# Performance work log

Measured on AMD Instinct MI355X. Metric: run time of the kernel, lower is better.

The kernel has to match this reference:

```python
import jax, jax.numpy as jnp
import numpy as np

B, N, T, CIN, HID, EMB, K = 32, 256, 13, 2, 64, 10, 2


def setup_inputs() -> dict:
    key = jax.random.key(0)
    ks = jax.random.split(key, 24)
    r = lambda i, shape, s=1.0: jax.random.normal(ks[i], shape, jnp.float32) * s
    return {
        "times": jnp.arange(T, dtype=jnp.float32),
        # natural cubic spline coefficients: (B, N, T-1, CIN)
        "coeff_a": r(0, (B, N, T - 1, CIN)),
        "coeff_b": r(1, (B, N, T - 1, CIN), 0.1),
        "coeff_two_c": r(2, (B, N, T - 1, CIN), 0.1),
        "coeff_three_d": r(3, (B, N, T - 1, CIN), 0.1),
        # initial_h / initial_z linear layers (input -> hidden)
        "W_h": r(4, (CIN, HID), 0.5), "b_h": r(5, (HID,), 0.1),
        "W_z": r(6, (CIN, HID), 0.5), "b_z": r(7, (HID,), 0.1),
        # func_f (FinalTanh_f): linear_in, one hidden linear, linear_out -> hidden*input
        "Wf_in": r(8, (HID, HID), 0.1), "bf_in": r(9, (HID,), 0.05),
        "Wf_hid": r(10, (HID, HID), 0.1), "bf_hid": r(11, (HID,), 0.05),
        "Wf_out": r(12, (HID, HID * CIN), 0.1), "bf_out": r(13, (HID * CIN,), 0.05),
        # func_g (VectorField_g, g_type='agc')
        "Wg_in": r(14, (HID, HID), 0.1), "bg_in": r(15, (HID,), 0.05),
        "Eg": r(16, (N, EMB)),
        "W_pool": r(17, (EMB, K, HID, HID), 0.1),
        "b_pool": r(18, (EMB, HID), 0.1),
        "Wg_out": r(19, (HID, HID * CIN), 0.1), "bg_out": r(20, (HID * CIN,), 0.05),
    }


def reference(times, coeff_a, coeff_b, coeff_two_c, coeff_three_d,
              W_h, b_h, W_z, b_z,
              Wf_in, bf_in, Wf_hid, bf_hid, Wf_out, bf_out,
              Wg_in, bg_in, Eg, W_pool, b_pool, Wg_out, bg_out):
    maxidx = coeff_b.shape[-2] - 1

    def dX_dt(t):  # NaturalCubicSpline.derivative
        idx = jnp.clip(jnp.searchsorted(times, t, side='right') - 1, 0, maxidx)
        frac = t - times[idx]
        b = coeff_b[..., idx, :]
        c = coeff_two_c[..., idx, :]
        d = coeff_three_d[..., idx, :]
        return b + (c + d * frac) * frac  # (B, N, CIN)

    # adaptive graph conv (agc) static pieces, cheb_k = 2
    A = jax.nn.softmax(jax.nn.relu(Eg @ Eg.T), axis=1)          # (N, N)
    supports = jnp.stack([jnp.eye(N, dtype=A.dtype), A])        # (K, N, N)
    Wn = jnp.einsum('nd,dkio->nkio', Eg, W_pool)                # (N, K, HID, HID)
    bn = Eg @ b_pool                                            # (N, HID)

    def func_f(h):  # FinalTanh_f: MLP -> (B, N, HID, CIN) field
        x = jax.nn.relu(h @ Wf_in + bf_in)
        x = jax.nn.relu(x @ Wf_hid + bf_hid)
        x = (x @ Wf_out + bf_out).reshape(*x.shape[:-1], HID, CIN)
        return jnp.tanh(x)

    def func_g(z):  # VectorField_g with agc
        x = jax.nn.relu(z @ Wg_in + bg_in)                       # (B, N, HID)
        x_g = jnp.einsum('knm,bmc->bnkc', supports, x)           # (B, N, K, HID)
        x = jnp.einsum('bnki,nkio->bno', x_g, Wn) + bn           # (B, N, HID)
        x = (x @ Wg_out + bg_out).reshape(*x.shape[:-1], HID, CIN)
        return jnp.tanh(x)

    def vf(t, h, z):  # VectorField_g_dev of cdeint_gde_dev
        dX = dX_dt(t)                                            # (B, N, CIN)
        f = func_f(h)
        g = func_g(z)
        dh = jnp.einsum('bnhi,bni->bnh', f, dX)
        dz = jnp.einsum('bnhi,bni->bnh', g * f, dX)
        return dh, dz

    # spline.evaluate(times[0]) == coeff_a[..., 0, :] (frac = 0)
    x0 = coeff_a[..., 0, :]
    h0 = x0 @ W_h + b_h
    z0 = x0 @ W_z + b_z

    third = jnp.float32(1.0 / 3.0)

    def step(carry, ts):  # torchdiffeq 'rk4' (3/8 rule), one step per interval
        h, z = carry
        t0, t1 = ts
        dt = t1 - t0
        k1h, k1z = vf(t0, h, z)
        k2h, k2z = vf(t0 + dt * third, h + dt * third * k1h, z + dt * third * k1z)
        k3h, k3z = vf(t0 + dt * 2 * third, h + dt * (k2h - third * k1h), z + dt * (k2z - third * k1z))
        k4h, k4z = vf(t1, h + dt * (k1h - k2h + k3h), z + dt * (k1z - k2z + k3z))
        h = h + dt * 0.125 * (k1h + 3.0 * (k2h + k3h) + k4h)
        z = z + dt * 0.125 * (k1z + 3.0 * (k2z + k3z) + k4z)
        return (h, z), z

    ts = jnp.stack([times[:-1], times[1:]], axis=1)              # (T-1, 2)
    (_, _), z_seq = jax.lax.scan(step, (h0, z0), ts)
    z_t = jnp.concatenate([z0[None], z_seq], axis=0)             # (T, B, N, HID)
    return jnp.transpose(z_t, (1, 2, 0, 3))                      # (B, N, T, HID)
```

## Files before the change

### kernel.cpp

```cpp
#include <hip/hip_runtime.h>

typedef unsigned short ushort_t;
typedef unsigned int uint_t;

#define CW_OFF  0
#define A_OFF   524288
#define BN_OFF  786432
#define WN_OFF  851968
#define XB_OFF  5046272
#define H_OFF   7143424
#define Z_OFF   9240576
#define K1H_OFF 11337728
#define K1Z_OFF 13434880
#define K2H_OFF 15532032
#define K2Z_OFF 17629184
#define UH_OFF  19726336

#define F_X0     0
#define F_WH     16384
#define F_BH     16512
#define F_WZ     16576
#define F_BZ     16704
#define F_WFIN   16768
#define F_BFIN   20864
#define F_WFHID  20928
#define F_BFHID  25024
#define F_WFOUT  25088
#define F_BFOUT  33280
#define F_WGIN   33408
#define F_BGIN   37504
#define F_WGOUT  37568
#define F_BGOUT  45760
#define F_EG     45888
#define F_WPOOL  48448
#define F_BPOOL  130368

__device__ __forceinline__ float bfl(uint_t u){ union{uint_t i; float f;} c; c.i = u<<16; return c.f; }
__device__ __forceinline__ float bfh(uint_t u){ union{uint_t i; float f;} c; c.i = u & 0xffff0000u; return c.f; }
__device__ __forceinline__ float bf1(ushort_t u){ union{uint_t i; float f;} c; c.i = ((uint_t)u)<<16; return c.f; }
__device__ __forceinline__ uint_t f2bf(float x){
  uint_t u = __float_as_uint(x);
  uint_t r = u + 0x7fffu + ((u >> 16) & 1u);
  return r >> 16;
}
__device__ __forceinline__ float fast_tanh(float x){
  float e = __expf(2.0f*x);
  return 1.0f - 2.0f/(e+1.0f);
}
__device__ __forceinline__ bool inputs_are_f32(const void* times){
  return ((const uint_t*)times)[0] != 0x3F800000u;
}

__device__ __forceinline__ void dotf_4(const float* act, const float* W, int o0, float acc[4]) {
  const float4* a4 = (const float4*)act;
  #pragma unroll
  for (int i4 = 0; i4 < 16; ++i4) {
    float4 av4 = a4[i4];
    float av[4] = {av4.x, av4.y, av4.z, av4.w};
    #pragma unroll
    for (int ii = 0; ii < 4; ++ii) {
      float4 w = *(const float4*)(W + (i4*4+ii)*64 + o0);
      acc[0] += av[ii]*w.x; acc[1] += av[ii]*w.y;
      acc[2] += av[ii]*w.z; acc[3] += av[ii]*w.w;
    }
  }
}

__device__ __forceinline__ void dotf_8(const float* act, const float* W, int co0, float acc[8]) {
  const float4* a4 = (const float4*)act;
  #pragma unroll
  for (int i4 = 0; i4 < 16; ++i4) {
    float4 av4 = a4[i4];
    float av[4] = {av4.x, av4.y, av4.z, av4.w};
    #pragma unroll
    for (int ii = 0; ii < 4; ++ii) {
      const float* wp = W + (i4*4+ii)*128 + co0;
      float4 w0 = *(const float4*)(wp);
      float4 w1 = *(const float4*)(wp + 4);
      float a = av[ii];
      acc[0] += a*w0.x; acc[1] += a*w0.y; acc[2] += a*w0.z; acc[3] += a*w0.w;
      acc[4] += a*w1.x; acc[5] += a*w1.y; acc[6] += a*w1.z; acc[7] += a*w1.w;
    }
  }
}

__global__ __launch_bounds__(256) void k_conv(
    const void* times, const void* ca,
    const void* W_h, const void* b_h, const void* W_z, const void* b_z,
    const void* Wf_in, const void* bf_in, const void* Wf_hid, const void* bf_hid,
    const void* Wf_out, const void* bf_out, const void* Wg_in, const void* bg_in,
    const void* Wg_out, const void* bg_out, const void* Eg, const void* W_pool,
    const void* b_pool, char* __restrict__ wsb)
{
  const bool f32in = inputs_are_f32(times);
  float* F = (float*)(wsb + CW_OFF);
  if (blockIdx.x == 0) {
    for (int i = threadIdx.x; i < 16384; i += 256) {
      int si = (i >> 1)*24 + (i & 1);
      F[F_X0 + i] = f32in ? ((const float*)ca)[si] : bf1(((const ushort_t*)ca)[si]);
    }
    return;
  }
  const void* src = nullptr; int dst = 0, cnt = 0;
  switch (blockIdx.x) {
    case 1:  src = W_h;    dst = F_WH;    cnt = 128;   break;
    case 2:  src = b_h;    dst = F_BH;    cnt = 64;    break;
    case 3:  src = W_z;    dst = F_WZ;    cnt = 128;   break;
    case 4:  src = b_z;    dst = F_BZ;    cnt = 64;    break;
    case 5:  src = Wf_in;  dst = F_WFIN;  cnt = 4096;  break;
    case 6:  src = bf_in;  dst = F_BFIN;  cnt = 64;    break;
    case 7:  src = Wf_hid; dst = F_WFHID; cnt = 4096;  break;
    case 8:  src = bf_hid; dst = F_BFHID; cnt = 64;    break;
    case 9:  src = Wf_out; dst = F_WFOUT; cnt = 8192;  break;
    case 10: src = bf_out; dst = F_BFOUT; cnt = 128;   break;
    case 11: src = Wg_in;  dst = F_WGIN;  cnt = 4096;  break;
    case 12: src = bg_in;  dst = F_BGIN;  cnt = 64;    break;
    case 13: src = Wg_out; dst = F_WGOUT; cnt = 8192;  break;
    case 14: src = bg_out; dst = F_BGOUT; cnt = 128;   break;
    case 15: src = Eg;     dst = F_EG;    cnt = 2560;  break;
    case 16: src = W_pool; dst = F_WPOOL; cnt = 81920; break;
    default: src = b_pool; dst = F_BPOOL; cnt = 640;   break;
  }
  for (int i = threadIdx.x; i < cnt; i += 256)
    F[dst + i] = f32in ? ((const float*)src)[i] : bf1(((const ushort_t*)src)[i]);
}

__global__ __launch_bounds__(256) void k_A(char* __restrict__ wsb) {
  const float* F = (const float*)(wsb + CW_OFF);
  float* Aw = (float*)(wsb + A_OFF);
  float* bn = (float*)(wsb + BN_OFF);
  const int nrow = blockIdx.x;
  const int m = threadIdx.x;
  float eg_n[10];
  #pragma unroll
  for (int d = 0; d < 10; ++d) eg_n[d] = F[F_EG + nrow*10 + d];
  float dot = 0.f;
  #pragma unroll
  for (int d = 0; d < 10; ++d) dot += eg_n[d] * F[F_EG + m*10 + d];
  float v = fmaxf(dot, 0.f);
  __shared__ float red[256];
  red[m] = v; __syncthreads();
  for (int off = 128; off > 0; off >>= 1) {
    if (m < off) red[m] = fmaxf(red[m], red[m+off]);
    __syncthreads();
  }
  float vmax = red[0]; __syncthreads();
  float e = __expf(v - vmax);
  red[m] = e; __syncthreads();
  for (int off = 128; off > 0; off >>= 1) {
    if (m < off) red[m] += red[m+off];
    __syncthreads();
  }
  float ssum = red[0];
  Aw[nrow*256 + m] = e / ssum;
  if (m < 64) {
    float acc = 0.f;
    #pragma unroll
    for (int d = 0; d < 10; ++d) acc += eg_n[d] * F[F_BPOOL + d*64 + m];
    bn[nrow*64 + m] = acc;
  }
}

__global__ __launch_bounds__(256) void k_Wn(char* __restrict__ wsb) {
  const float* F = (const float*)(wsb + CW_OFF);
  ushort_t* Wn = (ushort_t*)(wsb + WN_OFF);
  int idx = blockIdx.x*256 + threadIdx.x;
  int o = idx & 63;
  int i = (idx >> 6) & 63;
  int k = (idx >> 12) & 1;
  int n = idx >> 13;
  float acc = 0.f;
  #pragma unroll
  for (int d = 0; d < 10; ++d)
    acc += F[F_EG + n*10 + d] * F[F_WPOOL + ((d*2 + k)*64 + i)*64 + o];
  Wn[idx] = (ushort_t)f2bf(acc);
}

__global__ __launch_bounds__(512) void k_init2(char* __restrict__ wsb, float* __restrict__ out) {
  const float* F = (const float*)(wsb + CW_OFF);
  float* H = (float*)(wsb + H_OFF);
  float* Z = (float*)(wsb + Z_OFF);
  ushort_t* X0 = (ushort_t*)(wsb + XB_OFF);

  const int tid = threadIdx.x;
  const int lr  = tid >> 4;
  const int o0  = (tid & 15) * 4;
  const int row = blockIdx.x * 32 + lr;

  __shared__ __align__(16) float sIn[32][68];

  float a0 = F[F_X0 + row*2 + 0];
  float a1 = F[F_X0 + row*2 + 1];
  float h[4], z[4];
  #pragma unroll
  for (int j = 0; j < 4; ++j) {
    h[j] = a0*F[F_WH + o0+j] + a1*F[F_WH + 64+o0+j] + F[F_BH + o0+j];
    z[j] = a0*F[F_WZ + o0+j] + a1*F[F_WZ + 64+o0+j] + F[F_BZ + o0+j];
  }
  *(float4*)(H + row*64 + o0) = make_float4(h[0],h[1],h[2],h[3]);
  *(float4*)(Z + row*64 + o0) = make_float4(z[0],z[1],z[2],z[3]);
  *(float4*)(out + (row*13)*64 + o0) = make_float4(z[0],z[1],z[2],z[3]);

  *(float4*)&sIn[lr][o0] = make_float4(z[0],z[1],z[2],z[3]);
  __syncthreads();
  float xr[4];
  { float4 bv = *(const float4*)(F + F_BGIN + o0);
    xr[0]=bv.x; xr[1]=bv.y; xr[2]=bv.z; xr[3]=bv.w; }
  dotf_4(&sIn[lr][0], F + F_WGIN, o0, xr);
  #pragma unroll
  for (int j=0;j<4;++j) xr[j] = fmaxf(xr[j], 0.f);
  { uint2 pk;
    pk.x = f2bf(xr[0]) | (f2bf(xr[1]) << 16);
    pk.y = f2bf(xr[2]) | (f2bf(xr[3]) << 16);
    *(uint2*)(X0 + row*64 + o0) = pk; }
}

__global__ __launch_bounds__(512) void k_stage(
    const void* __restrict__ times,
    const void* __restrict__ cbv, const void* __restrict__ ccv, const void* __restrict__ cdv,
    char* __restrict__ wsb, float* __restrict__ out, int vfc)
{
  const float* F  = (const float*)(wsb + CW_OFF);
  const float* Aw = (const float*)(wsb + A_OFF);
  const float* bn = (const float*)(wsb + BN_OFF);
  const ushort_t* Wn = (const ushort_t*)(wsb + WN_OFF);
  ushort_t* XB = (ushort_t*)(wsb + XB_OFF);
  float* H   = (float*)(wsb + H_OFF);
  float* Z   = (float*)(wsb + Z_OFF);
  float* K1h = (float*)(wsb + K1H_OFF);
  float* K1z = (float*)(wsb + K1Z_OFF);
  float* K2h = (float*)(wsb + K2H_OFF);
  float* K2z = (float*)(wsb + K2Z_OFF);
  float* UH  = (float*)(wsb + UH_OFF);
  const bool f32in = inputs_are_f32(times);

  const int s  = vfc >> 2;
  const int st = vfc & 3;
  const ushort_t* Xc = XB + (vfc & 1) * 524288;
  ushort_t*       Xn = XB + ((vfc + 1) & 1) * 524288;

  const int tid = threadIdx.x;
  const int lr  = tid >> 4;
  const int t16 = tid & 15;
  const int o0  = t16 * 4;
  const int co0 = o0 * 2;
  const int bb  = blockIdx.x >> 3;
  const int nr  = blockIdx.x & 7;
  const int n   = nr * 32 + lr;
  const int row = bb * 256 + n;

  __shared__ __align__(16) float sIn[32][68];
  __shared__ __align__(16) float sT [32][68];
  __shared__ __align__(16) float sX [32][68];
  __shared__ __align__(16) float xs [128][68];

  { uint2 w = *(const uint2*)(Xc + row*64 + o0);
    *(float4*)&sX[lr][o0] = make_float4(bfl(w.x), bfh(w.x), bfl(w.y), bfh(w.y)); }

  float y[4] = {0.f,0.f,0.f,0.f};
  const float* Arow = Aw + n*256;
  #pragma unroll 1
  for (int half = 0; half < 2; ++half) {
    __syncthreads();
    #pragma unroll
    for (int q = tid; q < 2048; q += 512) {
      int r = q >> 4, c4 = q & 15;
      uint2 w = *(const uint2*)(Xc + (bb*256 + half*128 + r)*64 + c4*4);
      *(float4*)&xs[r][c4*4] = make_float4(bfl(w.x), bfh(w.x), bfl(w.y), bfh(w.y));
    }
    __syncthreads();
    #pragma unroll 4
    for (int m4 = 0; m4 < 32; ++m4) {
      float4 av = *(const float4*)(Arow + half*128 + m4*4);
      float am[4] = {av.x, av.y, av.z, av.w};
      #pragma unroll
      for (int mm = 0; mm < 4; ++mm) {
        float4 xv = *(const float4*)&xs[m4*4+mm][o0];
        y[0] += am[mm]*xv.x; y[1] += am[mm]*xv.y;
        y[2] += am[mm]*xv.z; y[3] += am[mm]*xv.w;
      }
    }
  }

  __syncthreads();
  *(float4*)&sT[lr][o0] = make_float4(y[0],y[1],y[2],y[3]);
  __syncthreads();
  float og[4];
  { float4 bv = *(const float4*)(bn + n*64 + o0); og[0]=bv.x; og[1]=bv.y; og[2]=bv.z; og[3]=bv.w; }
  const ushort_t* W0 = Wn + n*8192;
  #pragma unroll
  for (int i4 = 0; i4 < 16; ++i4) {
    float4 xa = *(const float4*)&sX[lr][i4*4];
    float4 ya = *(const float4*)&sT[lr][i4*4];
    float xav[4]={xa.x,xa.y,xa.z,xa.w};
    float yav[4]={ya.x,ya.y,ya.z,ya.w};
    #pragma unroll
    for (int ii = 0; ii < 4; ++ii) {
      int i = i4*4 + ii;
      uint2 w0 = *(const uint2*)(W0 + i*64 + o0);
      uint2 w1 = *(const uint2*)(W0 + 4096 + i*64 + o0);
      og[0] += xav[ii]*bfl(w0.x) + yav[ii]*bfl(w1.x);
      og[1] += xav[ii]*bfh(w0.x) + yav[ii]*bfh(w1.x);
      og[2] += xav[ii]*bfl(w0.y) + yav[ii]*bfl(w1.y);
      og[3] += xav[ii]*bfh(w0.y) + yav[ii]*bfh(w1.y);
    }
  }
  *(float4*)&sIn[lr][o0] = make_float4(og[0],og[1],og[2],og[3]);
  __syncthreads();
  float go[8];
  { float4 b0 = *(const float4*)(F + F_BGOUT + co0);
    float4 b1 = *(const float4*)(F + F_BGOUT + co0 + 4);
    go[0]=b0.x; go[1]=b0.y; go[2]=b0.z; go[3]=b0.w;
    go[4]=b1.x; go[5]=b1.y; go[6]=b1.z; go[7]=b1.w; }
  dotf_8(&sIn[lr][0], F + F_WGOUT, co0, go);
  float g0[4], g1[4];
  #pragma unroll
  for (int j=0;j<4;++j){ g0[j]=fast_tanh(go[2*j]); g1[j]=fast_tanh(go[2*j+1]); }

  __syncthreads();
  { const float* UHsrc = (st == 0) ? H : UH;
    float4 uv = *(const float4*)(UHsrc + row*64 + o0);
    *(float4*)&sIn[lr][o0] = uv; }
  __syncthreads();
  float a1v[4];
  { float4 bv = *(const float4*)(F + F_BFIN + o0);
    a1v[0]=bv.x; a1v[1]=bv.y; a1v[2]=bv.z; a1v[3]=bv.w; }
  dotf_4(&sIn[lr][0], F + F_WFIN, o0, a1v);
  #pragma unroll
  for (int j=0;j<4;++j) a1v[j] = fmaxf(a1v[j], 0.f);
  *(float4*)&sT[lr][o0] = make_float4(a1v[0],a1v[1],a1v[2],a1v[3]);
  __syncthreads();
  float a2v[4];
  { float4 bv = *(const float4*)(F + F_BFHID + o0);
    a2v[0]=bv.x; a2v[1]=bv.y; a2v[2]=bv.z; a2v[3]=bv.w; }
  dotf_4(&sT[lr][0], F + F_WFHID, o0, a2v);
  #pragma unroll
  for (int j=0;j<4;++j) a2v[j] = fmaxf(a2v[j], 0.f);
  *(float4*)&sIn[lr][o0] = make_float4(a2v[0],a2v[1],a2v[2],a2v[3]);
  __syncthreads();
  float fo[8];
  { float4 b0 = *(const float4*)(F + F_BFOUT + co0);
    float4 b1 = *(const float4*)(F + F_BFOUT + co0 + 4);
    fo[0]=b0.x; fo[1]=b0.y; fo[2]=b0.z; fo[3]=b0.w;
    fo[4]=b1.x; fo[5]=b1.y; fo[6]=b1.z; fo[7]=b1.w; }
  dotf_8(&sIn[lr][0], F + F_WFOUT, co0, fo);
  float f0[4], f1[4];
  #pragma unroll
  for (int j=0;j<4;++j){ f0[j]=fast_tanh(fo[2*j]); f1[j]=fast_tanh(fo[2*j+1]); }

  int sidx; float frac;
  if (st == 0)      { sidx = s; frac = 0.f; }
  else if (st == 1) { sidx = s; frac = 0.33333334f; }
  else if (st == 2) { sidx = s; frac = 0.66666669f; }
  else              { sidx = (s < 11) ? s+1 : 11; frac = (s < 11) ? 0.f : 1.f; }
  float dX0, dX1;
  if (f32in) {
    float2 vb = *(const float2*)((const float*)cbv + (row*12 + sidx)*2);
    float2 vc = *(const float2*)((const float*)ccv + (row*12 + sidx)*2);
    float2 vd = *(const float2*)((const float*)cdv + (row*12 + sidx)*2);
    dX0 = vb.x + (vc.x + vd.x*frac)*frac;
    dX1 = vb.y + (vc.y + vd.y*frac)*frac;
  } else {
    uint_t vb = *(const uint_t*)((const ushort_t*)cbv + (row*12 + sidx)*2);
    uint_t vc = *(const uint_t*)((const ushort_t*)ccv + (row*12 + sidx)*2);
    uint_t vd = *(const uint_t*)((const ushort_t*)cdv + (row*12 + sidx)*2);
    dX0 = bfl(vb) + (bfl(vc) + bfl(vd)*frac)*frac;
    dX1 = bfh(vb) + (bfh(vc) + bfh(vd)*frac)*frac;
  }

  float dh[4], dz[4];
  #pragma unroll
  for (int j=0;j<4;++j){
    dh[j] = f0[j]*dX0 + f1[j]*dX1;
    dz[j] = g0[j]*f0[j]*dX0 + g1[j]*f1[j]*dX1;
  }

  float uh_n[4], uz_n[4];
  float4 hv = *(const float4*)(H + row*64 + o0);
  float4 zv = *(const float4*)(Z + row*64 + o0);
  float h[4] = {hv.x,hv.y,hv.z,hv.w};
  float z[4] = {zv.x,zv.y,zv.z,zv.w};

  if (st == 0) {
    *(float4*)(K1h + row*64 + o0) = make_float4(dh[0],dh[1],dh[2],dh[3]);
    *(float4*)(K1z + row*64 + o0) = make_float4(dz[0],dz[1],dz[2],dz[3]);
    #pragma unroll
    for (int j=0;j<4;++j){ uh_n[j]=h[j]+dh[j]*(1.f/3.f); uz_n[j]=z[j]+dz[j]*(1.f/3.f); }
  } else if (st == 1) {
    float4 k1hv = *(const float4*)(K1h + row*64 + o0);
    float4 k1zv = *(const float4*)(K1z + row*64 + o0);
    float k1hl[4]={k1hv.x,k1hv.y,k1hv.z,k1hv.w};
    float k1zl[4]={k1zv.x,k1zv.y,k1zv.z,k1zv.w};
    float Qh[4],Qz[4],Ph[4],Pz[4];
    #pragma unroll
    for (int j=0;j<4;++j){
      Qh[j]=k1hl[j]+3.f*dh[j]; Qz[j]=k1zl[j]+3.f*dz[j];
      Ph[j]=k1hl[j]-dh[j];     Pz[j]=k1zl[j]-dz[j];
      uh_n[j]=h[j]+dh[j]-k1hl[j]*(1.f/3.f);
      uz_n[j]=z[j]+dz[j]-k1zl[j]*(1.f/3.f);
    }
    *(float4*)(K1h + row*64 + o0) = make_float4(Qh[0],Qh[1],Qh[2],Qh[3]);
    *(float4*)(K1z + row*64 + o0) = make_float4(Qz[0],Qz[1],Qz[2],Qz[3]);
    *(float4*)(K2h + row*64 + o0) = make_float4(Ph[0],Ph[1],Ph[2],Ph[3]);
    *(float4*)(K2z + row*64 + o0) = make_float4(Pz[0],Pz[1],Pz[2],Pz[3]);
  } else if (st == 2) {
    float4 Qhv = *(const float4*)(K1h + row*64 + o0);
    float4 Qzv = *(const float4*)(K1z + row*64 + o0);
    float4 Phv = *(const float4*)(K2h + row*64 + o0);
    float4 Pzv = *(const float4*)(K2z + row*64 + o0);
    float Qh[4]={Qhv.x,Qhv.y,Qhv.z,Qhv.w}, Qz[4]={Qzv.x,Qzv.y,Qzv.z,Qzv.w};
    float Ph[4]={Phv.x,Phv.y,Phv.z,Phv.w}, Pz[4]={Pzv.x,Pzv.y,Pzv.z,Pzv.w};
    float Ah[4],Az[4];
    #pragma unroll
    for (int j=0;j<4;++j){
      Ah[j]=Qh[j]+3.f*dh[j]; Az[j]=Qz[j]+3.f*dz[j];
      uh_n[j]=h[j]+Ph[j]+dh[j];
      uz_n[j]=z[j]+Pz[j]+dz[j];
    }
    *(float4*)(K1h + row*64 + o0) = make_float4(Ah[0],Ah[1],Ah[2],Ah[3]);
    *(float4*)(K1z + row*64 + o0) = make_float4(Az[0],Az[1],Az[2],Az[3]);
  } else {
    float4 Ahv = *(const float4*)(K1h + row*64 + o0);
    float4 Azv = *(const float4*)(K1z + row*64 + o0);
    #pragma unroll
    for (int j=0;j<4;++j){
      float hn = h[j] + 0.125f*(((const float*)&Ahv)[j] + dh[j]);
      float zn = z[j] + 0.125f*(((const float*)&Azv)[j] + dz[j]);
      uh_n[j]=hn; uz_n[j]=zn;
    }
    *(float4*)(H + row*64 + o0) = make_float4(uh_n[0],uh_n[1],uh_n[2],uh_n[3]);
    *(float4*)(Z + row*64 + o0) = make_float4(uz_n[0],uz_n[1],uz_n[2],uz_n[3]);
    *(float4*)(out + (row*13 + s + 1)*64 + o0) = make_float4(uz_n[0],uz_n[1],uz_n[2],uz_n[3]);
  }

  if (vfc < 47) {
    *(float4*)(UH + row*64 + o0) = make_float4(uh_n[0],uh_n[1],uh_n[2],uh_n[3]);
    __syncthreads();
    *(float4*)&sIn[lr][o0] = make_float4(uz_n[0],uz_n[1],uz_n[2],uz_n[3]);
    __syncthreads();
    float xr[4];
    { float4 bv = *(const float4*)(F + F_BGIN + o0);
      xr[0]=bv.x; xr[1]=bv.y; xr[2]=bv.z; xr[3]=bv.w; }
    dotf_4(&sIn[lr][0], F + F_WGIN, o0, xr);
    #pragma unroll
    for (int j=0;j<4;++j) xr[j] = fmaxf(xr[j], 0.f);
    uint2 pk;
    pk.x = f2bf(xr[0]) | (f2bf(xr[1]) << 16);
    pk.y = f2bf(xr[2]) | (f2bf(xr[3]) << 16);
    *(uint2*)(Xn + row*64 + o0) = pk;
  }
}

extern "C" void kernel_launch(void* const* d_in, const int* in_sizes, int n_in,
                              void* d_out, int out_size, void* d_ws, size_t ws_size,
                              hipStream_t stream) {
  const void* times   = d_in[0];
  const void* coeff_a = d_in[1];
  const void* coeff_b = d_in[2];
  const void* coeff_c = d_in[3];
  const void* coeff_d = d_in[4];
  const void* W_h    = d_in[5];
  const void* b_h    = d_in[6];
  const void* W_z    = d_in[7];
  const void* b_z    = d_in[8];
  const void* Wf_in  = d_in[9];
  const void* bf_in  = d_in[10];
  const void* Wf_hid = d_in[11];
  const void* bf_hid = d_in[12];
  const void* Wf_out = d_in[13];
  const void* bf_out = d_in[14];
  const void* Wg_in  = d_in[15];
  const void* bg_in  = d_in[16];
  const void* Eg     = d_in[17];
  const void* W_pool = d_in[18];
  const void* b_pool = d_in[19];
  const void* Wg_out = d_in[20];
  const void* bg_out = d_in[21];

  char* wsb = (char*)d_ws;
  float* out = (float*)d_out;

  hipLaunchKernelGGL(k_conv, dim3(18), dim3(256), 0, stream,
                     times, coeff_a, W_h, b_h, W_z, b_z,
                     Wf_in, bf_in, Wf_hid, bf_hid, Wf_out, bf_out,
                     Wg_in, bg_in, Wg_out, bg_out, Eg, W_pool, b_pool, wsb);
  hipLaunchKernelGGL(k_A,  dim3(256),  dim3(256), 0, stream, wsb);
  hipLaunchKernelGGL(k_Wn, dim3(8192), dim3(256), 0, stream, wsb);
  hipLaunchKernelGGL(k_init2, dim3(256), dim3(512), 0, stream, wsb, out);
  for (int vfc = 0; vfc < 48; ++vfc) {
    hipLaunchKernelGGL(k_stage, dim3(256), dim3(512), 0, stream,
                       times, coeff_b, coeff_c, coeff_d, wsb, out, vfc);
  }
}
```

Before: 5.064 ms.

## Fuse all RK4 stages into one persistent kernel with per-batch atomic barriers

Replaces the 49 per-stage launches with a single persistent kernel of 256 blocks. RK state (h, z, k1, k2, intermediates) stays in registers instead of round-tripping through global buffers. Blocks of the same batch synchronise through an atomic counter barrier before the graph-conv mixing step. The MLP weights are also stored and read as bf16 to halve weight traffic. This removes launch overhead and state memory traffic, but depends on all 256 blocks being co-resident to avoid deadlock, and the bf16 weights add rounding error.

```diff
diff --git a/kernel.cpp b/kernel.cpp
--- a/kernel.cpp
+++ b/kernel.cpp
@@ -3,18 +3,13 @@
 typedef unsigned short ushort_t;
 typedef unsigned int uint_t;
 
-#define CW_OFF  0
-#define A_OFF   524288
-#define BN_OFF  786432
-#define WN_OFF  851968
-#define XB_OFF  5046272
-#define H_OFF   7143424
-#define Z_OFF   9240576
-#define K1H_OFF 11337728
-#define K1Z_OFF 13434880
-#define K2H_OFF 15532032
-#define K2Z_OFF 17629184
-#define UH_OFF  19726336
+#define BAR_OFF 0
+#define CW_OFF  2048
+#define BW_OFF  526336
+#define A_OFF   583680
+#define BN_OFF  845824
+#define WN_OFF  911360
+#define XB_OFF  5105664
 
 #define F_X0     0
 #define F_WH     16384
@@ -35,6 +30,12 @@
 #define F_WPOOL  48448
 #define F_BPOOL  130368
 
+#define BW_WFIN  0
+#define BW_WFHID 4096
+#define BW_WFOUT 8192
+#define BW_WGIN  16384
+#define BW_WGOUT 20480
+
 __device__ __forceinline__ float bfl(uint_t u){ union{uint_t i; float f;} c; c.i = u<<16; return c.f; }
 __device__ __forceinline__ float bfh(uint_t u){ union{uint_t i; float f;} c; c.i = u & 0xffff0000u; return c.f; }
 __device__ __forceinline__ float bf1(ushort_t u){ union{uint_t i; float f;} c; c.i = ((uint_t)u)<<16; return c.f; }
@@ -51,37 +52,52 @@
   return ((const uint_t*)times)[0] != 0x3F800000u;
 }
 
-__device__ __forceinline__ void dotf_4(const float* act, const float* W, int o0, float acc[4]) {
+__device__ __forceinline__ void dot64_4(const float* act, const ushort_t* W, int o0, float acc[4]) {
   const float4* a4 = (const float4*)act;
   #pragma unroll
   for (int i4 = 0; i4 < 16; ++i4) {
     float4 av4 = a4[i4];
     float av[4] = {av4.x, av4.y, av4.z, av4.w};
+    const ushort_t* wp = W + i4*4*64 + o0;
     #pragma unroll
     for (int ii = 0; ii < 4; ++ii) {
-      float4 w = *(const float4*)(W + (i4*4+ii)*64 + o0);
-      acc[0] += av[ii]*w.x; acc[1] += av[ii]*w.y;
-      acc[2] += av[ii]*w.z; acc[3] += av[ii]*w.w;
+      uint2 w = *(const uint2*)(wp + ii*64);
+      acc[0] += av[ii]*bfl(w.x);
+      acc[1] += av[ii]*bfh(w.x);
+      acc[2] += av[ii]*bfl(w.y);
+      acc[3] += av[ii]*bfh(w.y);
     }
   }
 }
 
-__device__ __forceinline__ void dotf_8(const float* act, const float* W, int co0, float acc[8]) {
+__device__ __forceinline__ void dot64_8(const float* act, const ushort_t* W, int co0, float acc[8]) {
   const float4* a4 = (const float4*)act;
   #pragma unroll
   for (int i4 = 0; i4 < 16; ++i4) {
     float4 av4 = a4[i4];
     float av[4] = {av4.x, av4.y, av4.z, av4.w};
+    const ushort_t* wp = W + i4*4*128 + co0;
     #pragma unroll
     for (int ii = 0; ii < 4; ++ii) {
-      const float* wp = W + (i4*4+ii)*128 + co0;
-      float4 w0 = *(const float4*)(wp);
-      float4 w1 = *(const float4*)(wp + 4);
+      uint4 w = *(const uint4*)(wp + ii*128);
       float a = av[ii];
-      acc[0] += a*w0.x; acc[1] += a*w0.y; acc[2] += a*w0.z; acc[3] += a*w0.w;
-      acc[4] += a*w1.x; acc[5] += a*w1.y; acc[6] += a*w1.z; acc[7] += a*w1.w;
+      acc[0] += a*bfl(w.x); acc[1] += a*bfh(w.x);
+      acc[2] += a*bfl(w.y); acc[3] += a*bfh(w.y);
+      acc[4] += a*bfl(w.z); acc[5] += a*bfh(w.z);
+      acc[6] += a*bfl(w.w); acc[7] += a*bfh(w.w);
     }
   }
+}
+
+__device__ __forceinline__ void batch_sync(uint_t* cnt, int gen) {
+  __syncthreads();
+  __threadfence();
+  if (threadIdx.x == 0) {
+    __hip_atomic_fetch_add(cnt, 1u, __ATOMIC_ACQ_REL, __HIP_MEMORY_SCOPE_AGENT);
+    while (__hip_atomic_load(cnt, __ATOMIC_ACQUIRE, __HIP_MEMORY_SCOPE_AGENT) < (uint_t)(8*gen)) {}
+  }
+  __syncthreads();
+  __threadfence();
 }
 
 __global__ __launch_bounds__(256) void k_conv(
@@ -94,6 +110,7 @@
 {
   const bool f32in = inputs_are_f32(times);
   float* F = (float*)(wsb + CW_OFF);
+  ushort_t* BW = (ushort_t*)(wsb + BW_OFF);
   if (blockIdx.x == 0) {
     for (int i = threadIdx.x; i < 16384; i += 256) {
       int si = (i >> 1)*24 + (i & 1);
@@ -101,36 +118,41 @@
     }
     return;
   }
-  const void* src = nullptr; int dst = 0, cnt = 0;
+  const void* src = nullptr; int dst = 0, cnt = 0, bdst = -1;
   switch (blockIdx.x) {
     case 1:  src = W_h;    dst = F_WH;    cnt = 128;   break;
     case 2:  src = b_h;    dst = F_BH;    cnt = 64;    break;
     case 3:  src = W_z;    dst = F_WZ;    cnt = 128;   break;
     case 4:  src = b_z;    dst = F_BZ;    cnt = 64;    break;
-    case 5:  src = Wf_in;  dst = F_WFIN;  cnt = 4096;  break;
+    case 5:  src = Wf_in;  dst = F_WFIN;  cnt = 4096;  bdst = BW_WFIN;  break;
     case 6:  src = bf_in;  dst = F_BFIN;  cnt = 64;    break;
-    case 7:  src = Wf_hid; dst = F_WFHID; cnt = 4096;  break;
+    case 7:  src = Wf_hid; dst = F_WFHID; cnt = 4096;  bdst = BW_WFHID; break;
     case 8:  src = bf_hid; dst = F_BFHID; cnt = 64;    break;
-    case 9:  src = Wf_out; dst = F_WFOUT; cnt = 8192;  break;
+    case 9:  src = Wf_out; dst = F_WFOUT; cnt = 8192;  bdst = BW_WFOUT; break;
     case 10: src = bf_out; dst = F_BFOUT; cnt = 128;   break;
-    case 11: src = Wg_in;  dst = F_WGIN;  cnt = 4096;  break;
+    case 11: src = Wg_in;  dst = F_WGIN;  cnt = 4096;  bdst = BW_WGIN;  break;
     case 12: src = bg_in;  dst = F_BGIN;  cnt = 64;    break;
-    case 13: src = Wg_out; dst = F_WGOUT; cnt = 8192;  break;
+    case 13: src = Wg_out; dst = F_WGOUT; cnt = 8192;  bdst = BW_WGOUT; break;
     case 14: src = bg_out; dst = F_BGOUT; cnt = 128;   break;
     case 15: src = Eg;     dst = F_EG;    cnt = 2560;  break;
     case 16: src = W_pool; dst = F_WPOOL; cnt = 81920; break;
     default: src = b_pool; dst = F_BPOOL; cnt = 640;   break;
   }
-  for (int i = threadIdx.x; i < cnt; i += 256)
-    F[dst + i] = f32in ? ((const float*)src)[i] : bf1(((const ushort_t*)src)[i]);
+  for (int i = threadIdx.x; i < cnt; i += 256) {
+    float v = f32in ? ((const float*)src)[i] : bf1(((const ushort_t*)src)[i]);
+    F[dst + i] = v;
+    if (bdst >= 0) BW[bdst + i] = (ushort_t)f2bf(v);
+  }
 }
 
 __global__ __launch_bounds__(256) void k_A(char* __restrict__ wsb) {
+  uint_t* bar = (uint_t*)(wsb + BAR_OFF);
   const float* F = (const float*)(wsb + CW_OFF);
   float* Aw = (float*)(wsb + A_OFF);
   float* bn = (float*)(wsb + BN_OFF);
   const int nrow = blockIdx.x;
   const int m = threadIdx.x;
+  if (nrow == 0 && m < 32) bar[m*16] = 0u;
   float eg_n[10];
   #pragma unroll
   for (int d = 0; d < 10; ++d) eg_n[d] = F[F_EG + nrow*10 + d];
@@ -176,68 +198,19 @@
   Wn[idx] = (ushort_t)f2bf(acc);
 }
 
-__global__ __launch_bounds__(512) void k_init2(char* __restrict__ wsb, float* __restrict__ out) {
-  const float* F = (const float*)(wsb + CW_OFF);
-  float* H = (float*)(wsb + H_OFF);
-  float* Z = (float*)(wsb + Z_OFF);
-  ushort_t* X0 = (ushort_t*)(wsb + XB_OFF);
-
-  const int tid = threadIdx.x;
-  const int lr  = tid >> 4;
-  const int o0  = (tid & 15) * 4;
-  const int row = blockIdx.x * 32 + lr;
-
-  __shared__ __align__(16) float sIn[32][68];
-
-  float a0 = F[F_X0 + row*2 + 0];
-  float a1 = F[F_X0 + row*2 + 1];
-  float h[4], z[4];
-  #pragma unroll
-  for (int j = 0; j < 4; ++j) {
-    h[j] = a0*F[F_WH + o0+j] + a1*F[F_WH + 64+o0+j] + F[F_BH + o0+j];
-    z[j] = a0*F[F_WZ + o0+j] + a1*F[F_WZ + 64+o0+j] + F[F_BZ + o0+j];
-  }
-  *(float4*)(H + row*64 + o0) = make_float4(h[0],h[1],h[2],h[3]);
-  *(float4*)(Z + row*64 + o0) = make_float4(z[0],z[1],z[2],z[3]);
-  *(float4*)(out + (row*13)*64 + o0) = make_float4(z[0],z[1],z[2],z[3]);
-
-  *(float4*)&sIn[lr][o0] = make_float4(z[0],z[1],z[2],z[3]);
-  __syncthreads();
-  float xr[4];
-  { float4 bv = *(const float4*)(F + F_BGIN + o0);
-    xr[0]=bv.x; xr[1]=bv.y; xr[2]=bv.z; xr[3]=bv.w; }
-  dotf_4(&sIn[lr][0], F + F_WGIN, o0, xr);
-  #pragma unroll
-  for (int j=0;j<4;++j) xr[j] = fmaxf(xr[j], 0.f);
-  { uint2 pk;
-    pk.x = f2bf(xr[0]) | (f2bf(xr[1]) << 16);
-    pk.y = f2bf(xr[2]) | (f2bf(xr[3]) << 16);
-    *(uint2*)(X0 + row*64 + o0) = pk; }
-}
-
-__global__ __launch_bounds__(512) void k_stage(
+__global__ __launch_bounds__(512) void k_main(
     const void* __restrict__ times,
     const void* __restrict__ cbv, const void* __restrict__ ccv, const void* __restrict__ cdv,
-    char* __restrict__ wsb, float* __restrict__ out, int vfc)
+    char* __restrict__ wsb, float* __restrict__ out)
 {
+  uint_t* bar = (uint_t*)(wsb + BAR_OFF);
   const float* F  = (const float*)(wsb + CW_OFF);
+  const ushort_t* BW = (const ushort_t*)(wsb + BW_OFF);
   const float* Aw = (const float*)(wsb + A_OFF);
   const float* bn = (const float*)(wsb + BN_OFF);
   const ushort_t* Wn = (const ushort_t*)(wsb + WN_OFF);
   ushort_t* XB = (ushort_t*)(wsb + XB_OFF);
-  float* H   = (float*)(wsb + H_OFF);
-  float* Z   = (float*)(wsb + Z_OFF);
-  float* K1h = (float*)(wsb + K1H_OFF);
-  float* K1z = (float*)(wsb + K1Z_OFF);
-  float* K2h = (float*)(wsb + K2H_OFF);
-  float* K2z = (float*)(wsb + K2Z_OFF);
-  float* UH  = (float*)(wsb + UH_OFF);
   const bool f32in = inputs_are_f32(times);
-
-  const int s  = vfc >> 2;
-  const int st = vfc & 3;
-  const ushort_t* Xc = XB + (vfc & 1) * 524288;
-  ushort_t*       Xn = XB + ((vfc + 1) & 1) * 524288;
 
   const int tid = threadIdx.x;
   const int lr  = tid >> 4;
@@ -248,206 +221,198 @@
   const int nr  = blockIdx.x & 7;
   const int n   = nr * 32 + lr;
   const int row = bb * 256 + n;
+  uint_t* cnt = bar + bb*16;
 
   __shared__ __align__(16) float sIn[32][68];
   __shared__ __align__(16) float sT [32][68];
   __shared__ __align__(16) float sX [32][68];
   __shared__ __align__(16) float xs [128][68];
 
-  { uint2 w = *(const uint2*)(Xc + row*64 + o0);
-    *(float4*)&sX[lr][o0] = make_float4(bfl(w.x), bfh(w.x), bfl(w.y), bfh(w.y)); }
-
-  float y[4] = {0.f,0.f,0.f,0.f};
-  const float* Arow = Aw + n*256;
+  float h[4], z[4];
+  {
+    float a0 = F[F_X0 + row*2 + 0];
+    float a1 = F[F_X0 + row*2 + 1];
+    #pragma unroll
+    for (int j = 0; j < 4; ++j) {
+      h[j] = a0*F[F_WH + o0+j] + a1*F[F_WH + 64+o0+j] + F[F_BH + o0+j];
+      z[j] = a0*F[F_WZ + o0+j] + a1*F[F_WZ + 64+o0+j] + F[F_BZ + o0+j];
+    }
+    *(float4*)(out + (row*13)*64 + o0) = make_float4(z[0],z[1],z[2],z[3]);
+  }
+
+  float k1h[4],k1z[4],k2h[4],k2z[4],uh[4],uz[4];
+  int gen = 0;
+
   #pragma unroll 1
-  for (int half = 0; half < 2; ++half) {
-    __syncthreads();
+  for (int s = 0; s < 12; ++s) {
     #pragma unroll
-    for (int q = tid; q < 2048; q += 512) {
-      int r = q >> 4, c4 = q & 15;
-      uint2 w = *(const uint2*)(Xc + (bb*256 + half*128 + r)*64 + c4*4);
-      *(float4*)&xs[r][c4*4] = make_float4(bfl(w.x), bfh(w.x), bfl(w.y), bfh(w.y));
-    }
-    __syncthreads();
-    #pragma unroll 4
-    for (int m4 = 0; m4 < 32; ++m4) {
-      float4 av = *(const float4*)(Arow + half*128 + m4*4);
-      float am[4] = {av.x, av.y, av.z, av.w};
-      #pragma unroll
-      for (int mm = 0; mm < 4; ++mm) {
-        float4 xv = *(const float4*)&xs[m4*4+mm][o0];
-        y[0] += am[mm]*xv.x; y[1] += am[mm]*xv.y;
-        y[2] += am[mm]*xv.z; y[3] += am[mm]*xv.w;
+    for (int j=0;j<4;++j){ uh[j]=h[j]; uz[j]=z[j]; }
+    #pragma unroll 1
+    for (int st = 0; st < 4; ++st) {
+      const int vfc = s*4 + st;
+      ushort_t* Xc = XB + (vfc & 1) * 524288;
+
+      __syncthreads();
+      *(float4*)&sIn[lr][o0] = make_float4(uz[0],uz[1],uz[2],uz[3]);
+      __syncthreads();
+
+      float xr[4];
+      { float4 bv = *(const float4*)(F + F_BGIN + o0);
+        xr[0]=bv.x; xr[1]=bv.y; xr[2]=bv.z; xr[3]=bv.w; }
+      dot64_4(&sIn[lr][0], BW + BW_WGIN, o0, xr);
+      #pragma unroll
+      for (int j=0;j<4;++j) xr[j] = fmaxf(xr[j], 0.f);
+      *(float4*)&sX[lr][o0] = make_float4(xr[0],xr[1],xr[2],xr[3]);
+      { uint2 pk;
+        pk.x = f2bf(xr[0]) | (f2bf(xr[1]) << 16);
+        pk.y = f2bf(xr[2]) | (f2bf(xr[3]) << 16);
+        *(uint2*)(Xc + row*64 + o0) = pk; }
+      __syncthreads();
+
+      *(float4*)&sIn[lr][o0] = make_float4(uh[0],uh[1],uh[2],uh[3]);
+      __syncthreads();
+      float a1v[4];
+      { float4 bv = *(const float4*)(F + F_BFIN + o0);
+        a1v[0]=bv.x; a1v[1]=bv.y; a1v[2]=bv.z; a1v[3]=bv.w; }
+      dot64_4(&sIn[lr][0], BW + BW_WFIN, o0, a1v);
+      #pragma unroll
+      for (int j=0;j<4;++j) a1v[j] = fmaxf(a1v[j], 0.f);
+      *(float4*)&sT[lr][o0] = make_float4(a1v[0],a1v[1],a1v[2],a1v[3]);
+      __syncthreads();
+      float a2v[4];
+      { float4 bv = *(const float4*)(F + F_BFHID + o0);
+        a2v[0]=bv.x; a2v[1]=bv.y; a2v[2]=bv.z; a2v[3]=bv.w; }
+      dot64_4(&sT[lr][0], BW + BW_WFHID, o0, a2v);
+      #pragma unroll
+      for (int j=0;j<4;++j) a2v[j] = fmaxf(a2v[j], 0.f);
+      *(float4*)&sIn[lr][o0] = make_float4(a2v[0],a2v[1],a2v[2],a2v[3]);
+      __syncthreads();
+      float fo[8];
+      { float4 b0 = *(const float4*)(F + F_BFOUT + co0);
+        float4 b1 = *(const float4*)(F + F_BFOUT + co0 + 4);
+        fo[0]=b0.x; fo[1]=b0.y; fo[2]=b0.z; fo[3]=b0.w;
+        fo[4]=b1.x; fo[5]=b1.y; fo[6]=b1.z; fo[7]=b1.w; }
+      dot64_8(&sIn[lr][0], BW + BW_WFOUT, co0, fo);
+      float f0[4], f1[4];
+      #pragma unroll
+      for (int j=0;j<4;++j){ f0[j]=fast_tanh(fo[2*j]); f1[j]=fast_tanh(fo[2*j+1]); }
+
+      ++gen;
+      batch_sync(cnt, gen);
+
+      float y[4] = {0.f,0.f,0.f,0.f};
+      const float* Arow = Aw + n*256;
+      #pragma unroll 1
+      for (int half = 0; half < 2; ++half) {
+        #pragma unroll
+        for (int q = tid; q < 2048; q += 512) {
+          int r = q >> 4, c4 = q & 15;
+          uint2 w = *(const uint2*)(Xc + (bb*256 + half*128 + r)*64 + c4*4);
+          *(float4*)&xs[r][c4*4] = make_float4(bfl(w.x), bfh(w.x), bfl(w.y), bfh(w.y));
+        }
+        __syncthreads();
+        #pragma unroll 4
+        for (int m4 = 0; m4 < 32; ++m4) {
+          float4 av = *(const float4*)(Arow + half*128 + m4*4);
+          float am[4] = {av.x, av.y, av.z, av.w};
+          #pragma unroll
+          for (int mm = 0; mm < 4; ++mm) {
+            float4 xv = *(const float4*)&xs[m4*4+mm][o0];
+            y[0] += am[mm]*xv.x; y[1] += am[mm]*xv.y;
+            y[2] += am[mm]*xv.z; y[3] += am[mm]*xv.w;
+          }
+        }
+        __syncthreads();
+      }
+
+      *(float4*)&sT[lr][o0] = make_float4(y[0],y[1],y[2],y[3]);
+      __syncthreads();
+      float og[4];
+      { float4 bv = *(const float4*)(bn + n*64 + o0); og[0]=bv.x; og[1]=bv.y; og[2]=bv.z; og[3]=bv.w; }
+      const ushort_t* W0 = Wn + n*8192;
+      #pragma unroll
+      for (int i4 = 0; i4 < 16; ++i4) {
+        float4 xa = *(const float4*)&sX[lr][i4*4];
+        float4 ya = *(const float4*)&sT[lr][i4*4];
+        float xav[4]={xa.x,xa.y,xa.z,xa.w};
+        float yav[4]={ya.x,ya.y,ya.z,ya.w};
+        #pragma unroll
+        for (int ii = 0; ii < 4; ++ii) {
+          int i = i4*4 + ii;
+          uint2 w0 = *(const uint2*)(W0 + i*64 + o0);
+          uint2 w1 = *(const uint2*)(W0 + 4096 + i*64 + o0);
+          og[0] += xav[ii]*bfl(w0.x) + yav[ii]*bfl(w1.x);
+          og[1] += xav[ii]*bfh(w0.x) + yav[ii]*bfh(w1.x);
+          og[2] += xav[ii]*bfl(w0.y) + yav[ii]*bfl(w1.y);
+          og[3] += xav[ii]*bfh(w0.y) + yav[ii]*bfh(w1.y);
+        }
+      }
+      *(float4*)&sIn[lr][o0] = make_float4(og[0],og[1],og[2],og[3]);
+      __syncthreads();
+      float go[8];
+      { float4 b0 = *(const float4*)(F + F_BGOUT + co0);
+        float4 b1 = *(const float4*)(F + F_BGOUT + co0 + 4);
+        go[0]=b0.x; go[1]=b0.y; go[2]=b0.z; go[3]=b0.w;
+        go[4]=b1.x; go[5]=b1.y; go[6]=b1.z; go[7]=b1.w; }
+      dot64_8(&sIn[lr][0], BW + BW_WGOUT, co0, go);
+      float g0[4], g1[4];
+      #pragma unroll
+      for (int j=0;j<4;++j){ g0[j]=fast_tanh(go[2*j]); g1[j]=fast_tanh(go[2*j+1]); }
+
+      int sidx; float frac;
+      if (st == 0)      { sidx = s; frac = 0.f; }
+      else if (st == 1) { sidx = s; frac = 0.33333334f; }
+      else if (st == 2) { sidx = s; frac = 0.66666669f; }
+      else              { sidx = (s < 11) ? s+1 : 11; frac = (s < 11) ? 0.f : 1.f; }
+      float dX0, dX1;
+      if (f32in) {
+        float2 vb = *(const float2*)((const float*)cbv + (row*12 + sidx)*2);
+        float2 vc = *(const float2*)((const float*)ccv + (row*12 + sidx)*2);
+        float2 vd = *(const float2*)((const float*)cdv + (row*12 + sidx)*2);
+        dX0 = vb.x + (vc.x + vd.x*frac)*frac;
+        dX1 = vb.y + (vc.y + vd.y*frac)*frac;
+      } else {
+        uint_t vb = *(const uint_t*)((const ushort_t*)cbv + (row*12 + sidx)*2);
+        uint_t vc = *(const uint_t*)((const ushort_t*)ccv + (row*12 + sidx)*2);
+        uint_t vd = *(const uint_t*)((const ushort_t*)cdv + (row*12 + sidx)*2);
+        dX0 = bfl(vb) + (bfl(vc) + bfl(vd)*frac)*frac;
+        dX1 = bfh(vb) + (bfh(vc) + bfh(vd)*frac)*frac;
+      }
+
+      float dh[4], dz[4];
+      #pragma unroll
+      for (int j=0;j<4;++j){
+        dh[j] = f0[j]*dX0 + f1[j]*dX1;
+        dz[j] = g0[j]*f0[j]*dX0 + g1[j]*f1[j]*dX1;
+      }
+
+      if (st == 0) {
+        #pragma unroll
+        for (int j=0;j<4;++j){
+          k1h[j]=dh[j]; k1z[j]=dz[j];
+          uh[j]=h[j]+dh[j]*(1.f/3.f); uz[j]=z[j]+dz[j]*(1.f/3.f);
+        }
+      } else if (st == 1) {
+        #pragma unroll
+        for (int j=0;j<4;++j){
+          k2h[j]=dh[j]; k2z[j]=dz[j];
+          uh[j]=h[j]+dh[j]-k1h[j]*(1.f/3.f); uz[j]=z[j]+dz[j]-k1z[j]*(1.f/3.f);
+        }
+      } else if (st == 2) {
+        #pragma unroll
+        for (int j=0;j<4;++j){
+          uh[j]=h[j]+k1h[j]-k2h[j]+dh[j];  uz[j]=z[j]+k1z[j]-k2z[j]+dz[j];
+          k1h[j]=k1h[j]+3.f*(k2h[j]+dh[j]); k1z[j]=k1z[j]+3.f*(k2z[j]+dz[j]);
+        }
+      } else {
+        #pragma unroll
+        for (int j=0;j<4;++j){
+          h[j] += 0.125f*(k1h[j]+dh[j]);
+          z[j] += 0.125f*(k1z[j]+dz[j]);
+        }
+        *(float4*)(out + (row*13 + s + 1)*64 + o0) = make_float4(z[0],z[1],z[2],z[3]);
       }
     }
-  }
-
-  __syncthreads();
-  *(float4*)&sT[lr][o0] = make_float4(y[0],y[1],y[2],y[3]);
-  __syncthreads();
-  float og[4];
-  { float4 bv = *(const float4*)(bn + n*64 + o0); og[0]=bv.x; og[1]=bv.y; og[2]=bv.z; og[3]=bv.w; }
-  const ushort_t* W0 = Wn + n*8192;
-  #pragma unroll
-  for (int i4 = 0; i4 < 16; ++i4) {
-    float4 xa = *(const float4*)&sX[lr][i4*4];
-    float4 ya = *(const float4*)&sT[lr][i4*4];
-    float xav[4]={xa.x,xa.y,xa.z,xa.w};
-    float yav[4]={ya.x,ya.y,ya.z,ya.w};
-    #pragma unroll
-    for (int ii = 0; ii < 4; ++ii) {
-      int i = i4*4 + ii;
-      uint2 w0 = *(const uint2*)(W0 + i*64 + o0);
-      uint2 w1 = *(const uint2*)(W0 + 4096 + i*64 + o0);
-      og[0] += xav[ii]*bfl(w0.x) + yav[ii]*bfl(w1.x);
-      og[1] += xav[ii]*bfh(w0.x) + yav[ii]*bfh(w1.x);
-      og[2] += xav[ii]*bfl(w0.y) + yav[ii]*bfl(w1.y);
-      og[3] += xav[ii]*bfh(w0.y) + yav[ii]*bfh(w1.y);
-    }
-  }
-  *(float4*)&sIn[lr][o0] = make_float4(og[0],og[1],og[2],og[3]);
-  __syncthreads();
-  float go[8];
-  { float4 b0 = *(const float4*)(F + F_BGOUT + co0);
-    float4 b1 = *(const float4*)(F + F_BGOUT + co0 + 4);
-    go[0]=b0.x; go[1]=b0.y; go[2]=b0.z; go[3]=b0.w;
-    go[4]=b1.x; go[5]=b1.y; go[6]=b1.z; go[7]=b1.w; }
-  dotf_8(&sIn[lr][0], F + F_WGOUT, co0, go);
-  float g0[4], g1[4];
-  #pragma unroll
-  for (int j=0;j<4;++j){ g0[j]=fast_tanh(go[2*j]); g1[j]=fast_tanh(go[2*j+1]); }
-
-  __syncthreads();
-  { const float* UHsrc = (st == 0) ? H : UH;
-    float4 uv = *(const float4*)(UHsrc + row*64 + o0);
-    *(float4*)&sIn[lr][o0] = uv; }
-  __syncthreads();
-  float a1v[4];
-  { float4 bv = *(const float4*)(F + F_BFIN + o0);
-    a1v[0]=bv.x; a1v[1]=bv.y; a1v[2]=bv.z; a1v[3]=bv.w; }
-  dotf_4(&sIn[lr][0], F + F_WFIN, o0, a1v);
-  #pragma unroll
-  for (int j=0;j<4;++j) a1v[j] = fmaxf(a1v[j], 0.f);
-  *(float4*)&sT[lr][o0] = make_float4(a1v[0],a1v[1],a1v[2],a1v[3]);
-  __syncthreads();
-  float a2v[4];
-  { float4 bv = *(const float4*)(F + F_BFHID + o0);
-    a2v[0]=bv.x; a2v[1]=bv.y; a2v[2]=bv.z; a2v[3]=bv.w; }
-  dotf_4(&sT[lr][0], F + F_WFHID, o0, a2v);
-  #pragma unroll
-  for (int j=0;j<4;++j) a2v[j] = fmaxf(a2v[j], 0.f);
-  *(float4*)&sIn[lr][o0] = make_float4(a2v[0],a2v[1],a2v[2],a2v[3]);
-  __syncthreads();
-  float fo[8];
-  { float4 b0 = *(const float4*)(F + F_BFOUT + co0);
-    float4 b1 = *(const float4*)(F + F_BFOUT + co0 + 4);
-    fo[0]=b0.x; fo[1]=b0.y; fo[2]=b0.z; fo[3]=b0.w;
-    fo[4]=b1.x; fo[5]=b1.y; fo[6]=b1.z; fo[7]=b1.w; }
-  dotf_8(&sIn[lr][0], F + F_WFOUT, co0, fo);
-  float f0[4], f1[4];
-  #pragma unroll
-  for (int j=0;j<4;++j){ f0[j]=fast_tanh(fo[2*j]); f1[j]=fast_tanh(fo[2*j+1]); }
-
-  int sidx; float frac;
-  if (st == 0)      { sidx = s; frac = 0.f; }
-  else if (st == 1) { sidx = s; frac = 0.33333334f; }
-  else if (st == 2) { sidx = s; frac = 0.66666669f; }
-  else              { sidx = (s < 11) ? s+1 : 11; frac = (s < 11) ? 0.f : 1.f; }
-  float dX0, dX1;
-  if (f32in) {
-    float2 vb = *(const float2*)((const float*)cbv + (row*12 + sidx)*2);
-    float2 vc = *(const float2*)((const float*)ccv + (row*12 + sidx)*2);
-    float2 vd = *(const float2*)((const float*)cdv + (row*12 + sidx)*2);
-    dX0 = vb.x + (vc.x + vd.x*frac)*frac;
-    dX1 = vb.y + (vc.y + vd.y*frac)*frac;
-  } else {
-    uint_t vb = *(const uint_t*)((const ushort_t*)cbv + (row*12 + sidx)*2);
-    uint_t vc = *(const uint_t*)((const ushort_t*)ccv + (row*12 + sidx)*2);
-    uint_t vd = *(const uint_t*)((const ushort_t*)cdv + (row*12 + sidx)*2);
-    dX0 = bfl(vb) + (bfl(vc) + bfl(vd)*frac)*frac;
-    dX1 = bfh(vb) + (bfh(vc) + bfh(vd)*frac)*frac;
-  }
-
-  float dh[4], dz[4];
-  #pragma unroll
-  for (int j=0;j<4;++j){
-    dh[j] = f0[j]*dX0 + f1[j]*dX1;
-    dz[j] = g0[j]*f0[j]*dX0 + g1[j]*f1[j]*dX1;
-  }
-
-  float uh_n[4], uz_n[4];
-  float4 hv = *(const float4*)(H + row*64 + o0);
-  float4 zv = *(const float4*)(Z + row*64 + o0);
-  float h[4] = {hv.x,hv.y,hv.z,hv.w};
-  float z[4] = {zv.x,zv.y,zv.z,zv.w};
-
-  if (st == 0) {
-    *(float4*)(K1h + row*64 + o0) = make_float4(dh[0],dh[1],dh[2],dh[3]);
-    *(float4*)(K1z + row*64 + o0) = make_float4(dz[0],dz[1],dz[2],dz[3]);
-    #pragma unroll
-    for (int j=0;j<4;++j){ uh_n[j]=h[j]+dh[j]*(1.f/3.f); uz_n[j]=z[j]+dz[j]*(1.f/3.f); }
-  } else if (st == 1) {
-    float4 k1hv = *(const float4*)(K1h + row*64 + o0);
-    float4 k1zv = *(const float4*)(K1z + row*64 + o0);
-    float k1hl[4]={k1hv.x,k1hv.y,k1hv.z,k1hv.w};
-    float k1zl[4]={k1zv.x,k1zv.y,k1zv.z,k1zv.w};
-    float Qh[4],Qz[4],Ph[4],Pz[4];
-    #pragma unroll
-    for (int j=0;j<4;++j){
-      Qh[j]=k1hl[j]+3.f*dh[j]; Qz[j]=k1zl[j]+3.f*dz[j];
-      Ph[j]=k1hl[j]-dh[j];     Pz[j]=k1zl[j]-dz[j];
-      uh_n[j]=h[j]+dh[j]-k1hl[j]*(1.f/3.f);
-      uz_n[j]=z[j]+dz[j]-k1zl[j]*(1.f/3.f);
-    }
-    *(float4*)(K1h + row*64 + o0) = make_float4(Qh[0],Qh[1],Qh[2],Qh[3]);
-    *(float4*)(K1z + row*64 + o0) = make_float4(Qz[0],Qz[1],Qz[2],Qz[3]);
-    *(float4*)(K2h + row*64 + o0) = make_float4(Ph[0],Ph[1],Ph[2],Ph[3]);
-    *(float4*)(K2z + row*64 + o0) = make_float4(Pz[0],Pz[1],Pz[2],Pz[3]);
-  } else if (st == 2) {
-    float4 Qhv = *(const float4*)(K1h + row*64 + o0);
-    float4 Qzv = *(const float4*)(K1z + row*64 + o0);
-    float4 Phv = *(const float4*)(K2h + row*64 + o0);
-    float4 Pzv = *(const float4*)(K2z + row*64 + o0);
-    float Qh[4]={Qhv.x,Qhv.y,Qhv.z,Qhv.w}, Qz[4]={Qzv.x,Qzv.y,Qzv.z,Qzv.w};
-    float Ph[4]={Phv.x,Phv.y,Phv.z,Phv.w}, Pz[4]={Pzv.x,Pzv.y,Pzv.z,Pzv.w};
-    float Ah[4],Az[4];
-    #pragma unroll
-    for (int j=0;j<4;++j){
-      Ah[j]=Qh[j]+3.f*dh[j]; Az[j]=Qz[j]+3.f*dz[j];
-      uh_n[j]=h[j]+Ph[j]+dh[j];
-      uz_n[j]=z[j]+Pz[j]+dz[j];
-    }
-    *(float4*)(K1h + row*64 + o0) = make_float4(Ah[0],Ah[1],Ah[2],Ah[3]);
-    *(float4*)(K1z + row*64 + o0) = make_float4(Az[0],Az[1],Az[2],Az[3]);
-  } else {
-    float4 Ahv = *(const float4*)(K1h + row*64 + o0);
-    float4 Azv = *(const float4*)(K1z + row*64 + o0);
-    #pragma unroll
-    for (int j=0;j<4;++j){
-      float hn = h[j] + 0.125f*(((const float*)&Ahv)[j] + dh[j]);
-      float zn = z[j] + 0.125f*(((const float*)&Azv)[j] + dz[j]);
-      uh_n[j]=hn; uz_n[j]=zn;
-    }
-    *(float4*)(H + row*64 + o0) = make_float4(uh_n[0],uh_n[1],uh_n[2],uh_n[3]);
-    *(float4*)(Z + row*64 + o0) = make_float4(uz_n[0],uz_n[1],uz_n[2],uz_n[3]);
-    *(float4*)(out + (row*13 + s + 1)*64 + o0) = make_float4(uz_n[0],uz_n[1],uz_n[2],uz_n[3]);
-  }
-
-  if (vfc < 47) {
-    *(float4*)(UH + row*64 + o0) = make_float4(uh_n[0],uh_n[1],uh_n[2],uh_n[3]);
-    __syncthreads();
-    *(float4*)&sIn[lr][o0] = make_float4(uz_n[0],uz_n[1],uz_n[2],uz_n[3]);
-    __syncthreads();
-    float xr[4];
-    { float4 bv = *(const float4*)(F + F_BGIN + o0);
-      xr[0]=bv.x; xr[1]=bv.y; xr[2]=bv.z; xr[3]=bv.w; }
-    dotf_4(&sIn[lr][0], F + F_WGIN, o0, xr);
-    #pragma unroll
-    for (int j=0;j<4;++j) xr[j] = fmaxf(xr[j], 0.f);
-    uint2 pk;
-    pk.x = f2bf(xr[0]) | (f2bf(xr[1]) << 16);
-    pk.y = f2bf(xr[2]) | (f2bf(xr[3]) << 16);
-    *(uint2*)(Xn + row*64 + o0) = pk;
   }
 }
 
@@ -486,9 +451,6 @@
                      Wg_in, bg_in, Wg_out, bg_out, Eg, W_pool, b_pool, wsb);
   hipLaunchKernelGGL(k_A,  dim3(256),  dim3(256), 0, stream, wsb);
   hipLaunchKernelGGL(k_Wn, dim3(8192), dim3(256), 0, stream, wsb);
-  hipLaunchKernelGGL(k_init2, dim3(256), dim3(512), 0, stream, wsb, out);
-  for (int vfc = 0; vfc < 48; ++vfc) {
-    hipLaunchKernelGGL(k_stage, dim3(256), dim3(512), 0, stream,
-                       times, coeff_b, coeff_c, coeff_d, wsb, out, vfc);
-  }
-}
+  hipLaunchKernelGGL(k_main, dim3(256), dim3(512), 0, stream,
+                     times, coeff_b, coeff_c, coeff_d, wsb, out);
+}
```

Result: slower. 17.83 ms (+252.0%).
